# Optimization experiments

Measured on AMD Instinct MI355X. Metric: run time of the kernel, lower is better.

Reference implementation:

```python
import jax, jax.numpy as jnp
import numpy as np

T, B, N_IN, N_HID, N_OUT = 32, 32, 512, 1024, 256

def _xavier(key, fan_in, fan_out):
    scale = jnp.sqrt(2.0 / (fan_in + fan_out)).astype(jnp.float32)
    return jax.random.normal(key, (fan_in, fan_out), dtype=jnp.float32) * scale

def setup_inputs() -> dict:
    key = jax.random.key(0)
    ks = jax.random.split(key, 8)
    return {
        'x_in': jax.random.normal(ks[0], (T, B, N_IN), dtype=jnp.float32),
        'W_i': _xavier(ks[1], N_IN, N_HID),
        'W_z': _xavier(ks[2], N_HID, N_HID),
        'W_c': _xavier(ks[3], N_HID, N_HID),
        'W_h': _xavier(ks[4], N_HID, N_HID),
        'W_ho': _xavier(ks[5], N_HID, N_HID),
        'W_o': _xavier(ks[6], N_HID, N_OUT),
        'lam': jnp.array([0.9], dtype=jnp.float32),
        'eta': jnp.array([0.5], dtype=jnp.float32),
        'g': jnp.ones((1, N_HID), dtype=jnp.float32),
        'b': jnp.ones((1, N_HID), dtype=jnp.float32),
        'mode': 0,
        'time': T,
    }

def reference(x_in, W_i, W_z, W_c, W_h, W_ho, W_o, lam, eta, g, b, mode, time):
    relu = jax.nn.relu
    n_steps = int(time)  # dt = 1.0
    batch, n_hidden = x_in.shape[1], W_i.shape[1]

    def step(carry, x_t):
        h, a = carry
        x = relu(x_t)                              # [B, n_in]
        s = relu(x @ W_i)                          # [B, H]
        z = relu(s @ W_z)                          # [B, H]
        zc = z @ W_c                               # reused twice
        h = relu(zc + h @ W_h)                     # [B, H]
        # fast-weight update: a <- lam*a + eta * h^T h (per-batch outer product)
        a = lam[0] * a + eta[0] * jnp.einsum('bi,bj->bij', h, h)  # [B, H, H]
        # one inner readout/normalization step
        hs = h @ W_h + zc + jnp.einsum('bk,bkj->bj', h, a)        # [B, H]
        mu = jnp.mean(hs, axis=0)                                 # [H]
        sig = jnp.sqrt(jnp.mean((hs - mu) ** 2, axis=0))          # [H] (biased std)
        hs = relu(g[0] * (hs - mu) / sig + b[0])
        return (hs, a), None

    h0 = jnp.zeros((batch, n_hidden), dtype=x_in.dtype)
    a0 = jnp.zeros((batch, n_hidden, n_hidden), dtype=x_in.dtype)
    (h, a), _ = jax.lax.scan(step, (h0, a0), x_in[:n_steps])

    o = relu(h @ W_ho)
    y = relu(o @ W_o)
    return y.reshape(1, batch, -1)
```

## Files before the change

kernel.cpp:

```cpp
#include <hip/hip_runtime.h>
#include <hip/hip_bf16.h>

#define T_   32
#define B_   32
#define NIN_ 512
#define H_   1024
#define NOUT_ 256
#define NBLK 64
#define NTHR 1024
#define NCOL 16
#define NSLOT 80
#define PACKB 128
#define GBM 64
#define GBN 64
#define GBK 128

typedef short bf16x8 __attribute__((ext_vector_type(8)));
typedef float f32x4  __attribute__((ext_vector_type(4)));
typedef unsigned int u32x4 __attribute__((ext_vector_type(4)));

__device__ __forceinline__ float bf2f(unsigned short u) {
  union { unsigned int i; float f; } x; x.i = ((unsigned int)u) << 16; return x.f;
}
__device__ __forceinline__ unsigned short f2bf(float f) {
  __hip_bfloat16 h = __float2bfloat16(f);
  return *reinterpret_cast<unsigned short*>(&h);
}
__device__ __forceinline__ unsigned int packf(float v) {
  unsigned short h = f2bf(v);
  unsigned short l = f2bf(v - bf2f(h));
  return ((unsigned int)h << 16) | l;
}
__device__ __forceinline__ void unpack8v(u32x4 a, u32x4 b, bf16x8& hi, bf16x8& lo) {
  unsigned int t[8] = {a[0], a[1], a[2], a[3], b[0], b[1], b[2], b[3]};
  union { bf16x8 v; unsigned int u[4]; } H, L;
#pragma unroll
  for (int j = 0; j < 4; j++) {
    unsigned int e = t[2 * j], o = t[2 * j + 1];
    H.u[j] = (o & 0xFFFF0000u) | (e >> 16);
    L.u[j] = (o << 16) | (e & 0xFFFFu);
  }
  hi = H.v; lo = L.v;
}

__device__ __forceinline__ void astu(unsigned int* p, unsigned int v) {
  __hip_atomic_store(p, v, __ATOMIC_RELAXED, __HIP_MEMORY_SCOPE_AGENT);
}
__device__ __forceinline__ void astf(float* p, float v) {
  __hip_atomic_store(p, v, __ATOMIC_RELAXED, __HIP_MEMORY_SCOPE_AGENT);
}
__device__ __forceinline__ void aaddf(float* p, float v) {
  __hip_atomic_fetch_add(p, v, __ATOMIC_RELAXED, __HIP_MEMORY_SCOPE_AGENT);
}

__device__ __forceinline__ void rendezvous(int* cnt, int slot) {
  __syncthreads();
  if (threadIdx.x == 0) {
    __hip_atomic_fetch_add(&cnt[slot], 1, __ATOMIC_RELAXED, __HIP_MEMORY_SCOPE_AGENT);
    while (__hip_atomic_load(&cnt[slot], __ATOMIC_RELAXED, __HIP_MEMORY_SCOPE_AGENT) < NBLK)
      __builtin_amdgcn_s_sleep(1);
    __atomic_signal_fence(__ATOMIC_ACQUIRE);
  }
  __syncthreads();
}

__global__ void init_detect(const unsigned short* __restrict__ x_raw,
                            int* __restrict__ flag, int* __restrict__ cnt) {
  __shared__ int bad;
  if (threadIdx.x == 0) bad = 0;
  __syncthreads();
  int c = 0;
  for (int i = threadIdx.x; i < 2048; i += 256) {
    float v = bf2f(x_raw[i]);
    if (!(fabsf(v) < 1e9f)) c++;
  }
  if (c) atomicAdd(&bad, 1);
  __syncthreads();
  if (threadIdx.x == 0) flag[0] = bad ? 1 : 0;
  for (int i = threadIdx.x; i < NSLOT; i += 256)
    __hip_atomic_store(&cnt[i], 0, __ATOMIC_RELAXED, __HIP_MEMORY_SCOPE_AGENT);
}

__global__ void prep_all(
    const void* __restrict__ x_in, unsigned int* __restrict__ X_pk,
    const void* lam, const void* eta, const void* g, const void* b,
    float* __restrict__ par,
    const void* __restrict__ W_i,  unsigned short* __restrict__ WiT_hi,  unsigned short* __restrict__ WiT_lo,
    const void* __restrict__ W_z,  unsigned short* __restrict__ WzT_hi,  unsigned short* __restrict__ WzT_lo,
    const void* __restrict__ W_c,  unsigned short* __restrict__ WcT_hi,  unsigned short* __restrict__ WcT_lo,
    const void* __restrict__ W_h,  unsigned short* __restrict__ WhT_hi,  unsigned short* __restrict__ WhT_lo,
    const void* __restrict__ W_ho, unsigned short* __restrict__ WhoT_hi, unsigned short* __restrict__ WhoT_lo,
    const void* __restrict__ W_o,  unsigned short* __restrict__ WoT_hi,  unsigned short* __restrict__ WoT_lo,
    const int* __restrict__ flag)
{
  const bool isf32 = flag[0] != 0;
  int blk = blockIdx.x;
  if (blk < PACKB) {
    const int n = T_ * B_ * NIN_;
    for (int i = blk * 256 + threadIdx.x; i < n; i += PACKB * 256) {
      float v = isf32 ? ((const float*)x_in)[i] : bf2f(((const unsigned short*)x_in)[i]);
      X_pk[i] = packf(fmaxf(v, 0.f));
    }
    return;
  }
  blk -= PACKB;
  if (blk < 4) {
    int t = blk * 256 + threadIdx.x;
    if (t == 0) {
      par[0] = isf32 ? ((const float*)lam)[0] : bf2f(((const unsigned short*)lam)[0]);
      par[1] = isf32 ? ((const float*)eta)[0] : bf2f(((const unsigned short*)eta)[0]);
    }
    if (t < H_) {
      par[2 + t]      = isf32 ? ((const float*)g)[t] : bf2f(((const unsigned short*)g)[t]);
      par[2 + H_ + t] = isf32 ? ((const float*)b)[t] : bf2f(((const unsigned short*)b)[t]);
    }
    return;
  }
  blk -= 4;
  const void* src; unsigned short *dhi, *dlo; int R, C;
  int tb = blk;
  if (tb < 512)       { src = W_i;  dhi = WiT_hi;  dlo = WiT_lo;  R = NIN_; C = H_; }
  else if (tb < 1536) { tb -= 512;  src = W_z;  dhi = WzT_hi;  dlo = WzT_lo;  R = H_; C = H_; }
  else if (tb < 2560) { tb -= 1536; src = W_c;  dhi = WcT_hi;  dlo = WcT_lo;  R = H_; C = H_; }
  else if (tb < 3584) { tb -= 2560; src = W_h;  dhi = WhT_hi;  dlo = WhT_lo;  R = H_; C = H_; }
  else if (tb < 4608) { tb -= 3584; src = W_ho; dhi = WhoT_hi; dlo = WhoT_lo; R = H_; C = H_; }
  else                { tb -= 4608; src = W_o;  dhi = WoT_hi;  dlo = WoT_lo;  R = H_; C = NOUT_; }
  __shared__ unsigned short thi[32][33], tlo[32][33];
  int ncx = C >> 5;
  int c0 = (tb % ncx) * 32, r0 = (tb / ncx) * 32;
  int tx = threadIdx.x & 31, ty = threadIdx.x >> 5;
  for (int i = ty; i < 32; i += 8) {
    size_t idx = (size_t)(r0 + i) * C + c0 + tx;
    float v = isf32 ? ((const float*)src)[idx] : bf2f(((const unsigned short*)src)[idx]);
    unsigned short h = f2bf(v);
    thi[i][tx] = h;
    tlo[i][tx] = f2bf(v - bf2f(h));
  }
  __syncthreads();
  for (int i = ty; i < 32; i += 8) {
    dhi[(size_t)(c0 + i) * R + r0 + tx] = thi[tx][i];
    dlo[(size_t)(c0 + i) * R + r0 + tx] = tlo[tx][i];
  }
}

template<int K, int OUTMODE>
__global__ void __launch_bounds__(1024) gemmT(
    const unsigned int* __restrict__ A,
    const unsigned short* __restrict__ BT_hi,
    const unsigned short* __restrict__ BT_lo,
    void* __restrict__ C) {
  __shared__ unsigned int   As[GBM][GBK + 4];
  __shared__ unsigned short Bh[GBN][GBK + 8];
  __shared__ unsigned short Bl[GBN][GBK + 8];
  const int tid = threadIdx.x;
  const int wv = tid >> 6, lane = tid & 63;
  const int col = lane & 15, quad = lane >> 4;
  const int wr = wv >> 2, wc = wv & 3;
  const int bm0 = (blockIdx.x >> 4) * GBM;
  const int bn0 = (blockIdx.x & 15) * GBN;
  const int sr = tid >> 4;
  const int sc = (tid & 15) * 8;
  f32x4 acc = {0.f, 0.f, 0.f, 0.f};
#pragma unroll 1
  for (int k0 = 0; k0 < K; k0 += GBK) {
    const unsigned int* ga = A + (size_t)(bm0 + sr) * K + k0 + sc;
    u32x4 a0 = *(const u32x4*)ga;
    u32x4 a1 = *(const u32x4*)(ga + 4);
    bf16x8 vh = *(const bf16x8*)(BT_hi + (size_t)(bn0 + sr) * K + k0 + sc);
    bf16x8 vl = *(const bf16x8*)(BT_lo + (size_t)(bn0 + sr) * K + k0 + sc);
    *(u32x4*)&As[sr][sc]     = a0;
    *(u32x4*)&As[sr][sc + 4] = a1;
    *(bf16x8*)&Bh[sr][sc] = vh;
    *(bf16x8*)&Bl[sr][sc] = vl;
    __syncthreads();
#pragma unroll
    for (int s = 0; s < GBK; s += 32) {
      bf16x8 ahi, alo;
      u32x4 c0v = *(const u32x4*)&As[wr * 16 + col][s + quad * 8];
      u32x4 c1v = *(const u32x4*)&As[wr * 16 + col][s + quad * 8 + 4];
      unpack8v(c0v, c1v, ahi, alo);
      bf16x8 bh8 = *(const bf16x8*)&Bh[wc * 16 + col][s + quad * 8];
      bf16x8 bl8 = *(const bf16x8*)&Bl[wc * 16 + col][s + quad * 8];
      acc = __builtin_amdgcn_mfma_f32_16x16x32_bf16(ahi, bh8, acc, 0, 0, 0);
      acc = __builtin_amdgcn_mfma_f32_16x16x32_bf16(alo, bh8, acc, 0, 0, 0);
      acc = __builtin_amdgcn_mfma_f32_16x16x32_bf16(ahi, bl8, acc, 0, 0, 0);
    }
    __syncthreads();
  }
#pragma unroll
  for (int r = 0; r < 4; r++) {
    size_t idx = (size_t)(bm0 + wr * 16 + quad * 4 + r) * H_ + bn0 + wc * 16 + col;
    if (OUTMODE) ((unsigned int*)C)[idx] = packf(fmaxf(acc[r], 0.f));
    else         ((float*)C)[idx] = acc[r];
  }
}

template<int NIT>
__device__ __forceinline__ f32x4 mm_partN(
    const unsigned int* __restrict__ A, int am0, int k0,
    const unsigned short* __restrict__ BH, const unsigned short* __restrict__ BL,
    int bj0, int col, int quad) {
  const unsigned int*   ap = A  + (size_t)(am0 + col) * H_ + k0 + quad * 8;
  const unsigned short* bh = BH + (size_t)(bj0 + col) * H_ + k0 + quad * 8;
  const unsigned short* bl = BL + (size_t)(bj0 + col) * H_ + k0 + quad * 8;
  u32x4 ab[2 * NIT];
#pragma unroll
  for (int i = 0; i < NIT; i++) {
    ab[2 * i]     = *(const u32x4*)(ap + 32 * i);
    ab[2 * i + 1] = *(const u32x4*)(ap + 32 * i + 4);
  }
  f32x4 acc = {0.f, 0.f, 0.f, 0.f};
#pragma unroll
  for (int i = 0; i < NIT; i++) {
    bf16x8 ahi, alo;
    unpack8v(ab[2 * i], ab[2 * i + 1], ahi, alo);
    bf16x8 vh = *(const bf16x8*)(bh + 32 * i);
    bf16x8 vl = *(const bf16x8*)(bl + 32 * i);
    acc = __builtin_amdgcn_mfma_f32_16x16x32_bf16(ahi, vh, acc, 0, 0, 0);
    acc = __builtin_amdgcn_mfma_f32_16x16x32_bf16(alo, vh, acc, 0, 0, 0);
    acc = __builtin_amdgcn_mfma_f32_16x16x32_bf16(ahi, vl, acc, 0, 0, 0);
  }
  return acc;
}
__device__ __forceinline__ f32x4 mm_tile_pf(
    const unsigned int* __restrict__ A, int am0,
    const unsigned short* __restrict__ BH, const unsigned short* __restrict__ BL,
    int bj0, f32x4 acc, int col, int quad) {
#pragma unroll 1
  for (int kk = 0; kk < H_; kk += 256) {
    f32x4 p = mm_partN<8>(A, am0, kk, BH, BL, bj0, col, quad);
    acc[0] += p[0]; acc[1] += p[1]; acc[2] += p[2]; acc[3] += p[3];
  }
  return acc;
}

__global__ void __launch_bounds__(NTHR) recurrent(
    const unsigned short* __restrict__ WhT_hi, const unsigned short* __restrict__ WhT_lo,
    const unsigned short* __restrict__ WhoT_hi, const unsigned short* __restrict__ WhoT_lo,
    const unsigned short* __restrict__ WoT_hi, const unsigned short* __restrict__ WoT_lo,
    const float* __restrict__ ZC,
    unsigned int* __restrict__ hq,
    unsigned int* __restrict__ hc,
    unsigned int* __restrict__ Opub,
    float* __restrict__ hist_loc,
    float* __restrict__ dots_g,
    const float* __restrict__ par,
    void* __restrict__ y_out,
    int* __restrict__ cnt,
    const int* __restrict__ flag)
{
  __shared__ f32x4 red[16][64];
  __shared__ float lds_hs[B_][NCOL + 1];
  __shared__ float lds_dt[B_][T_];
  __shared__ float lds_mu[NCOL], lds_sc[NCOL], lds_bb[NCOL];

  const int tid = threadIdx.x, wg = blockIdx.x;
  const int wv = tid >> 6, lane = tid & 63;
  const int col = lane & 15, quad = lane >> 4;
  const int j0 = wg * NCOL;
  const int tile = wv & 1, kp = wv >> 1;
  const int am0 = tile * 16;
  const int k0 = kp * 128;
  const float lam = par[0], eta = par[1];
  const bool isf32 = flag[0] != 0;
  float* hl = hist_loc + (size_t)wg * (T_ * B_ * NCOL);

  for (int d = tid; d < B_ * NCOL; d += NTHR) {
    int b = d >> 4, c = d & 15;
    astu(hc + (size_t)b * H_ + j0 + c, 0u);
  }
  for (int i = tid; i < T_ * B_ * T_ / NBLK; i += NTHR)
    astf(dots_g + (size_t)wg * (T_ * B_ * T_ / NBLK) + i, 0.f);
  rendezvous(cnt, 0);

  int slot = 1;
  for (int t = 0; t < T_; ++t) {
    const float* zb = ZC + (size_t)t * B_ * H_;
    const unsigned int* hcur = hc + (size_t)t * B_ * H_;
    unsigned int* hqt = hq + (size_t)t * B_ * H_;
    float* dt = dots_g + (size_t)t * B_ * T_;
    red[wv][lane] = mm_partN<4>(hcur, am0, k0, WhT_hi, WhT_lo, j0, col, quad);
    __syncthreads();
    if (wv < 2) {
      int a0 = wv * 16;
      f32x4 s = red[wv][lane];
#pragma unroll
      for (int k = 1; k < 8; k++) {
        f32x4 p = red[wv + 2 * k][lane];
        s[0] += p[0]; s[1] += p[1]; s[2] += p[2]; s[3] += p[3];
      }
#pragma unroll
      for (int r = 0; r < 4; r++) {
        float v = zb[(size_t)(a0 + quad * 4 + r) * H_ + j0 + col] + s[r];
        v = fmaxf(v, 0.f);
        int m = a0 + quad * 4 + r;
        hl[((size_t)t * B_ + m) * NCOL + col] = v;
        astu(hqt + (size_t)m * H_ + j0 + col, packf(v));
      }
    }
    __syncthreads();
    for (int d = tid; d < B_ * (t + 1); d += NTHR) {
      int b = ((d / (t + 1)) + wg) & (B_ - 1);
      int s = d % (t + 1);
      const f32x4* p = (const f32x4*)(hl + ((size_t)t * B_ + b) * NCOL);
      const f32x4* q = (const f32x4*)(hl + ((size_t)s * B_ + b) * NCOL);
      float sum = 0.f;
#pragma unroll
      for (int i = 0; i < 4; i++) {
        f32x4 a = p[i], c = q[i];
        sum += a[0] * c[0] + a[1] * c[1] + a[2] * c[2] + a[3] * c[3];
      }
      aaddf(dt + (size_t)b * T_ + s, sum);
    }
    rendezvous(cnt, slot++);
    for (int d = tid; d < B_ * (t + 1); d += NTHR) {
      int b = d / (t + 1), s = d - b * (t + 1);
      lds_dt[b][s] = dt[(size_t)b * T_ + s];
    }
    red[wv][lane] = mm_partN<4>(hqt, am0, k0, WhT_hi, WhT_lo, j0, col, quad);
    __syncthreads();
    if (wv < 2) {
      int a0 = wv * 16;
      f32x4 s = red[wv][lane];
#pragma unroll
      for (int k = 1; k < 8; k++) {
        f32x4 p = red[wv + 2 * k][lane];
        s[0] += p[0]; s[1] += p[1]; s[2] += p[2]; s[3] += p[3];
      }
#pragma unroll
      for (int r = 0; r < 4; r++)
        lds_hs[a0 + quad * 4 + r][col] =
            zb[(size_t)(a0 + quad * 4 + r) * H_ + j0 + col] + s[r];
    }
    __syncthreads();
    for (int d = tid; d < B_ * NCOL; d += NTHR) {
      int b = d >> 4, c = d & 15;
      float a = 0.f, w = eta;
      const float* hb = hl + (size_t)b * NCOL + c;
      for (int s = t; s >= 0; --s) {
        a += w * lds_dt[b][s] * hb[(size_t)s * B_ * NCOL];
        w *= lam;
      }
      lds_hs[b][c] += a;
    }
    __syncthreads();
    if (tid < NCOL) {
      int c = tid;
      float sum = 0.f;
#pragma unroll
      for (int b = 0; b < B_; b++) sum += lds_hs[b][c];
      float mu = sum * (1.f / B_);
      float sq = 0.f;
#pragma unroll
      for (int b = 0; b < B_; b++) {
        float dd = lds_hs[b][c] - mu;
        sq += dd * dd;
      }
      float sig = sqrtf(sq * (1.f / B_));
      lds_mu[c] = mu;
      lds_sc[c] = par[2 + j0 + c] / sig;
      lds_bb[c] = par[2 + H_ + j0 + c];
    }
    __syncthreads();
    for (int d = tid; d < B_ * NCOL; d += NTHR) {
      int b = d >> 4, c = d & 15;
      float v = (lds_hs[b][c] - lds_mu[c]) * lds_sc[c] + lds_bb[c];
      astu(hc + (size_t)(t + 1) * B_ * H_ + (size_t)b * H_ + j0 + c, packf(fmaxf(v, 0.f)));
    }
    rendezvous(cnt, slot++);
  }
  {
    const unsigned int* hfin = hc + (size_t)T_ * B_ * H_;
    red[wv][lane] = mm_partN<4>(hfin, am0, k0, WhoT_hi, WhoT_lo, j0, col, quad);
    __syncthreads();
    if (wv < 2) {
      int a0 = wv * 16;
      f32x4 s = red[wv][lane];
#pragma unroll
      for (int k = 1; k < 8; k++) {
        f32x4 p = red[wv + 2 * k][lane];
        s[0] += p[0]; s[1] += p[1]; s[2] += p[2]; s[3] += p[3];
      }
#pragma unroll
      for (int r = 0; r < 4; r++) {
        float v = fmaxf(s[r], 0.f);
        astu(Opub + (size_t)(a0 + quad * 4 + r) * H_ + j0 + col, packf(v));
      }
    }
  }
  rendezvous(cnt, slot++);
  if (wg < 2) {
    int id = wg * 16 + wv;
    int bt2 = id & 1, jt2 = id >> 1;
    f32x4 acc = {0.f, 0.f, 0.f, 0.f};
    acc = mm_tile_pf(Opub, bt2 * 16, WoT_hi, WoT_lo, jt2 * 16, acc, col, quad);
#pragma unroll
    for (int r = 0; r < 4; r++) {
      float v = fmaxf(acc[r], 0.f);
      size_t idx = (size_t)(bt2 * 16 + quad * 4 + r) * NOUT_ + jt2 * 16 + col;
      if (isf32) ((float*)y_out)[idx] = v;
      else       ((unsigned short*)y_out)[idx] = f2bf(v);
    }
  }
}

extern "C" void kernel_launch(void* const* d_in, const int* in_sizes, int n_in,
                              void* d_out, int out_size, void* d_ws, size_t ws_size,
                              hipStream_t stream) {
  const void* x_in = d_in[0];
  const void* W_i  = d_in[1];
  const void* W_z  = d_in[2];
  const void* W_c  = d_in[3];
  const void* W_h  = d_in[4];
  const void* W_ho = d_in[5];
  const void* W_o  = d_in[6];
  const void* lam  = d_in[7];
  const void* eta  = d_in[8];
  const void* g    = d_in[9];
  const void* bb   = d_in[10];

  char* wsp = (char*)d_ws;
  size_t off = 0;
  auto alloc = [&](size_t bytes) {
    void* p = wsp + off;
    off += (bytes + 255) & ~(size_t)255;
    return p;
  };
  int*            flag    = (int*)alloc(16);
  int*            cnt     = (int*)alloc(NSLOT * 4);
  float*          par     = (float*)alloc((2 + 2 * H_) * 4);
  unsigned int*   X_pk    = (unsigned int*)alloc((size_t)T_ * B_ * NIN_ * 4);
  unsigned short* WiT_hi  = (unsigned short*)alloc((size_t)NIN_ * H_ * 2);
  unsigned short* WiT_lo  = (unsigned short*)alloc((size_t)NIN_ * H_ * 2);
  unsigned short* WzT_hi  = (unsigned short*)alloc((size_t)H_ * H_ * 2);
  unsigned short* WzT_lo  = (unsigned short*)alloc((size_t)H_ * H_ * 2);
  unsigned short* WcT_hi  = (unsigned short*)alloc((size_t)H_ * H_ * 2);
  unsigned short* WcT_lo  = (unsigned short*)alloc((size_t)H_ * H_ * 2);
  unsigned short* WhT_hi  = (unsigned short*)alloc((size_t)H_ * H_ * 2);
  unsigned short* WhT_lo  = (unsigned short*)alloc((size_t)H_ * H_ * 2);
  unsigned short* WhoT_hi = (unsigned short*)alloc((size_t)H_ * H_ * 2);
  unsigned short* WhoT_lo = (unsigned short*)alloc((size_t)H_ * H_ * 2);
  unsigned short* WoT_hi  = (unsigned short*)alloc((size_t)H_ * NOUT_ * 2);
  unsigned short* WoT_lo  = (unsigned short*)alloc((size_t)H_ * NOUT_ * 2);
  unsigned int*   S_pk    = (unsigned int*)alloc((size_t)T_ * B_ * H_ * 4);
  unsigned int*   Z_pk    = (unsigned int*)alloc((size_t)T_ * B_ * H_ * 4);
  float*          ZC      = (float*)alloc((size_t)T_ * B_ * H_ * 4);
  unsigned int*   hq      = (unsigned int*)alloc((size_t)T_ * B_ * H_ * 4);
  unsigned int*   hc      = (unsigned int*)alloc((size_t)(T_ + 1) * B_ * H_ * 4);
  unsigned int*   Opub    = (unsigned int*)alloc((size_t)B_ * H_ * 4);
  float*          histloc = (float*)alloc((size_t)NBLK * T_ * B_ * NCOL * 4);
  float*          dots_g  = (float*)alloc((size_t)T_ * B_ * T_ * 4);
  (void)ws_size; (void)in_sizes; (void)n_in; (void)out_size;

  init_detect<<<1, 256, 0, stream>>>((const unsigned short*)x_in, flag, cnt);

  prep_all<<<PACKB + 4 + 4864, 256, 0, stream>>>(
      x_in, X_pk, lam, eta, g, bb, par,
      W_i, WiT_hi, WiT_lo, W_z, WzT_hi, WzT_lo, W_c, WcT_hi, WcT_lo,
      W_h, WhT_hi, WhT_lo, W_ho, WhoT_hi, WhoT_lo, W_o, WoT_hi, WoT_lo,
      flag);

  gemmT<NIN_, 1><<<256, 1024, 0, stream>>>(X_pk, WiT_hi, WiT_lo, S_pk);
  gemmT<H_,   1><<<256, 1024, 0, stream>>>(S_pk, WzT_hi, WzT_lo, Z_pk);
  gemmT<H_,   0><<<256, 1024, 0, stream>>>(Z_pk, WcT_hi, WcT_lo, ZC);

  recurrent<<<NBLK, NTHR, 0, stream>>>(WhT_hi, WhT_lo, WhoT_hi, WhoT_lo, WoT_hi, WoT_lo,
                                       ZC, hq, hc, Opub, histloc, dots_g,
                                       par, d_out, cnt, flag);
}
```

Baseline: 725.3 us.

## Retile pre-GEMMs with register prefetch and fold dtype detection into prep

The precomputation GEMMs now use 128x64 tiles with K-step 64. Each wave computes two 16x16 tiles, so one B fragment serves two M sub-tiles, and the next K tile is prefetched into registers while the current one is computed. Grid size halves to 128 blocks. The separate init_detect launch is removed: each prep_all block repeats the dtype probe itself and block 0 resets the counters. This trades one kernel launch for redundant probing in every block, and fewer blocks may leave CUs idle.

```diff
diff --git a/kernel.cpp b/kernel.cpp
--- a/kernel.cpp
+++ b/kernel.cpp
@@ -11,13 +11,14 @@
 #define NCOL 16
 #define NSLOT 80
 #define PACKB 128
-#define GBM 64
+#define GBM 128
 #define GBN 64
-#define GBK 128
+#define GBK 64
 
 typedef short bf16x8 __attribute__((ext_vector_type(8)));
 typedef float f32x4  __attribute__((ext_vector_type(4)));
 typedef unsigned int u32x4 __attribute__((ext_vector_type(4)));
+typedef unsigned short u16x4 __attribute__((ext_vector_type(4)));
 
 __device__ __forceinline__ float bf2f(unsigned short u) {
   union { unsigned int i; float f; } x; x.i = ((unsigned int)u) << 16; return x.f;
@@ -62,23 +63,6 @@
     __atomic_signal_fence(__ATOMIC_ACQUIRE);
   }
   __syncthreads();
-}
-
-__global__ void init_detect(const unsigned short* __restrict__ x_raw,
-                            int* __restrict__ flag, int* __restrict__ cnt) {
-  __shared__ int bad;
-  if (threadIdx.x == 0) bad = 0;
-  __syncthreads();
-  int c = 0;
-  for (int i = threadIdx.x; i < 2048; i += 256) {
-    float v = bf2f(x_raw[i]);
-    if (!(fabsf(v) < 1e9f)) c++;
-  }
-  if (c) atomicAdd(&bad, 1);
-  __syncthreads();
-  if (threadIdx.x == 0) flag[0] = bad ? 1 : 0;
-  for (int i = threadIdx.x; i < NSLOT; i += 256)
-    __hip_atomic_store(&cnt[i], 0, __ATOMIC_RELAXED, __HIP_MEMORY_SCOPE_AGENT);
 }
 
 __global__ void prep_all(
@@ -91,9 +75,27 @@
     const void* __restrict__ W_h,  unsigned short* __restrict__ WhT_hi,  unsigned short* __restrict__ WhT_lo,
     const void* __restrict__ W_ho, unsigned short* __restrict__ WhoT_hi, unsigned short* __restrict__ WhoT_lo,
     const void* __restrict__ W_o,  unsigned short* __restrict__ WoT_hi,  unsigned short* __restrict__ WoT_lo,
-    const int* __restrict__ flag)
+    int* __restrict__ flag, int* __restrict__ cnt)
 {
-  const bool isf32 = flag[0] != 0;
+  __shared__ int bad;
+  if (threadIdx.x == 0) bad = 0;
+  __syncthreads();
+  {
+    const unsigned short* xr = (const unsigned short*)x_in;
+    int c = 0;
+    for (int i = threadIdx.x; i < 2048; i += 256) {
+      float v = bf2f(xr[i]);
+      if (!(fabsf(v) < 1e9f)) c++;
+    }
+    if (c) atomicAdd(&bad, 1);
+  }
+  __syncthreads();
+  const bool isf32 = bad != 0;
+  if (blockIdx.x == 0) {
+    if (threadIdx.x == 0) flag[0] = isf32 ? 1 : 0;
+    if (threadIdx.x < NSLOT)
+      __hip_atomic_store(&cnt[threadIdx.x], 0, __ATOMIC_RELAXED, __HIP_MEMORY_SCOPE_AGENT);
+  }
   int blk = blockIdx.x;
   if (blk < PACKB) {
     const int n = T_ * B_ * NIN_;
@@ -155,43 +157,61 @@
   const int tid = threadIdx.x;
   const int wv = tid >> 6, lane = tid & 63;
   const int col = lane & 15, quad = lane >> 4;
-  const int wr = wv >> 2, wc = wv & 3;
+  const int mt = (wv >> 2) * 2;
+  const int nt = wv & 3;
   const int bm0 = (blockIdx.x >> 4) * GBM;
   const int bn0 = (blockIdx.x & 15) * GBN;
-  const int sr = tid >> 4;
-  const int sc = (tid & 15) * 8;
-  f32x4 acc = {0.f, 0.f, 0.f, 0.f};
+  const int ar = tid >> 3, ac = (tid & 7) * 8;
+  const int br = tid >> 4, bc = (tid & 15) * 4;
+  f32x4 acc0 = {0.f, 0.f, 0.f, 0.f}, acc1 = {0.f, 0.f, 0.f, 0.f};
+  u32x4 ra0 = *(const u32x4*)(A + (size_t)(bm0 + ar) * K + ac);
+  u32x4 ra1 = *(const u32x4*)(A + (size_t)(bm0 + ar) * K + ac + 4);
+  u16x4 rbh = *(const u16x4*)(BT_hi + (size_t)(bn0 + br) * K + bc);
+  u16x4 rbl = *(const u16x4*)(BT_lo + (size_t)(bn0 + br) * K + bc);
 #pragma unroll 1
   for (int k0 = 0; k0 < K; k0 += GBK) {
-    const unsigned int* ga = A + (size_t)(bm0 + sr) * K + k0 + sc;
-    u32x4 a0 = *(const u32x4*)ga;
-    u32x4 a1 = *(const u32x4*)(ga + 4);
-    bf16x8 vh = *(const bf16x8*)(BT_hi + (size_t)(bn0 + sr) * K + k0 + sc);
-    bf16x8 vl = *(const bf16x8*)(BT_lo + (size_t)(bn0 + sr) * K + k0 + sc);
-    *(u32x4*)&As[sr][sc]     = a0;
-    *(u32x4*)&As[sr][sc + 4] = a1;
-    *(bf16x8*)&Bh[sr][sc] = vh;
-    *(bf16x8*)&Bl[sr][sc] = vl;
-    __syncthreads();
+    *(u32x4*)&As[ar][ac]     = ra0;
+    *(u32x4*)&As[ar][ac + 4] = ra1;
+    *(u16x4*)&Bh[br][bc] = rbh;
+    *(u16x4*)&Bl[br][bc] = rbl;
+    __syncthreads();
+    if (k0 + GBK < K) {
+      ra0 = *(const u32x4*)(A + (size_t)(bm0 + ar) * K + k0 + GBK + ac);
+      ra1 = *(const u32x4*)(A + (size_t)(bm0 + ar) * K + k0 + GBK + ac + 4);
+      rbh = *(const u16x4*)(BT_hi + (size_t)(bn0 + br) * K + k0 + GBK + bc);
+      rbl = *(const u16x4*)(BT_lo + (size_t)(bn0 + br) * K + k0 + GBK + bc);
+    }
 #pragma unroll
     for (int s = 0; s < GBK; s += 32) {
+      bf16x8 bh8 = *(const bf16x8*)&Bh[nt * 16 + col][s + quad * 8];
+      bf16x8 bl8 = *(const bf16x8*)&Bl[nt * 16 + col][s + quad * 8];
       bf16x8 ahi, alo;
-      u32x4 c0v = *(const u32x4*)&As[wr * 16 + col][s + quad * 8];
-      u32x4 c1v = *(const u32x4*)&As[wr * 16 + col][s + quad * 8 + 4];
+      u32x4 c0v = *(const u32x4*)&As[mt * 16 + col][s + quad * 8];
+      u32x4 c1v = *(const u32x4*)&As[mt * 16 + col][s + quad * 8 + 4];
       unpack8v(c0v, c1v, ahi, alo);
-      bf16x8 bh8 = *(const bf16x8*)&Bh[wc * 16 + col][s + quad * 8];
-      bf16x8 bl8 = *(const bf16x8*)&Bl[wc * 16 + col][s + quad * 8];
-      acc = __builtin_amdgcn_mfma_f32_16x16x32_bf16(ahi, bh8, acc, 0, 0, 0);
-      acc = __builtin_amdgcn_mfma_f32_16x16x32_bf16(alo, bh8, acc, 0, 0, 0);
-      acc = __builtin_amdgcn_mfma_f32_16x16x32_bf16(ahi, bl8, acc, 0, 0, 0);
+      acc0 = __builtin_amdgcn_mfma_f32_16x16x32_bf16(ahi, bh8, acc0, 0, 0, 0);
+      acc0 = __builtin_amdgcn_mfma_f32_16x16x32_bf16(alo, bh8, acc0, 0, 0, 0);
+      acc0 = __builtin_amdgcn_mfma_f32_16x16x32_bf16(ahi, bl8, acc0, 0, 0, 0);
+      u32x4 d0v = *(const u32x4*)&As[(mt + 1) * 16 + col][s + quad * 8];
+      u32x4 d1v = *(const u32x4*)&As[(mt + 1) * 16 + col][s + quad * 8 + 4];
+      unpack8v(d0v, d1v, ahi, alo);
+      acc1 = __builtin_amdgcn_mfma_f32_16x16x32_bf16(ahi, bh8, acc1, 0, 0, 0);
+      acc1 = __builtin_amdgcn_mfma_f32_16x16x32_bf16(alo, bh8, acc1, 0, 0, 0);
+      acc1 = __builtin_amdgcn_mfma_f32_16x16x32_bf16(ahi, bl8, acc1, 0, 0, 0);
     }
     __syncthreads();
   }
 #pragma unroll
   for (int r = 0; r < 4; r++) {
-    size_t idx = (size_t)(bm0 + wr * 16 + quad * 4 + r) * H_ + bn0 + wc * 16 + col;
-    if (OUTMODE) ((unsigned int*)C)[idx] = packf(fmaxf(acc[r], 0.f));
-    else         ((float*)C)[idx] = acc[r];
+    size_t i0 = (size_t)(bm0 + mt * 16 + quad * 4 + r) * H_ + bn0 + nt * 16 + col;
+    size_t i1 = (size_t)(bm0 + (mt + 1) * 16 + quad * 4 + r) * H_ + bn0 + nt * 16 + col;
+    if (OUTMODE) {
+      ((unsigned int*)C)[i0] = packf(fmaxf(acc0[r], 0.f));
+      ((unsigned int*)C)[i1] = packf(fmaxf(acc1[r], 0.f));
+    } else {
+      ((float*)C)[i0] = acc0[r];
+      ((float*)C)[i1] = acc1[r];
+    }
   }
 }
 
@@ -452,17 +472,15 @@
   float*          dots_g  = (float*)alloc((size_t)T_ * B_ * T_ * 4);
   (void)ws_size; (void)in_sizes; (void)n_in; (void)out_size;
 
-  init_detect<<<1, 256, 0, stream>>>((const unsigned short*)x_in, flag, cnt);
-
   prep_all<<<PACKB + 4 + 4864, 256, 0, stream>>>(
       x_in, X_pk, lam, eta, g, bb, par,
       W_i, WiT_hi, WiT_lo, W_z, WzT_hi, WzT_lo, W_c, WcT_hi, WcT_lo,
       W_h, WhT_hi, WhT_lo, W_ho, WhoT_hi, WhoT_lo, W_o, WoT_hi, WoT_lo,
-      flag);
-
-  gemmT<NIN_, 1><<<256, 1024, 0, stream>>>(X_pk, WiT_hi, WiT_lo, S_pk);
-  gemmT<H_,   1><<<256, 1024, 0, stream>>>(S_pk, WzT_hi, WzT_lo, Z_pk);
-  gemmT<H_,   0><<<256, 1024, 0, stream>>>(Z_pk, WcT_hi, WcT_lo, ZC);
+      flag, cnt);
+
+  gemmT<NIN_, 1><<<128, 1024, 0, stream>>>(X_pk, WiT_hi, WiT_lo, S_pk);
+  gemmT<H_,   1><<<128, 1024, 0, stream>>>(S_pk, WzT_hi, WzT_lo, Z_pk);
+  gemmT<H_,   0><<<128, 1024, 0, stream>>>(Z_pk, WcT_hi, WcT_lo, ZC);
 
   recurrent<<<NBLK, NTHR, 0, stream>>>(WhT_hi, WhT_lo, WhoT_hi, WhoT_lo, WoT_hi, WoT_lo,
                                        ZC, hq, hc, Opub, histloc, dots_g,
```

New measurement: 736.8 us. Within noise of the previous version (+1.6%).
